# Performance work log

Hardware: AMD Instinct MI355X
Metric: run time of the kernel (lower is better)

## Reference

```python
import jax, jax.numpy as jnp
import numpy as np

EDGE = 255                      # env_edge_size
ADD = (EDGE - 1) // 2           # additional_size = 127
AX = EDGE + ADD                 # axial_size = 382 (input height H)
BATCH = 16
CHAN = 32


def setup_inputs() -> dict:
    key = jax.random.key(0)
    k1, k2 = jax.random.split(key)
    axial_tensor = jax.random.normal(k1, (BATCH, CHAN, AX, EDGE), dtype=jnp.float32)
    offset = jax.random.randint(k2, (BATCH, 2), 0, EDGE)  # (q, r) per batch
    return {"axial_tensor": axial_tensor, "offset": offset}


def reference(axial_tensor, offset):
    # Faithful translation of AxialTranslatorRotator.translate (translate=True path).
    B, C, H, W = axial_tensor.shape          # H = axial_size, W = edge_size
    add = H - W                              # additional_size
    S = 2 * H + 1                            # placeholder side = 2*axial_size + 1

    q = offset[:, 0]
    r = offset[:, 1]
    uoff = q - r // 2                        # us in torch code (floor div, r >= 0)

    # _axial_indices flatten order: loops over (u=i in [0,W), v=j in [0,H)),
    # flat index k = i*H + j; original gather reads x[b, c, j, i].
    j = jnp.arange(H)                        # v coordinate (indexes input H dim)
    i = jnp.arange(W)                        # u coordinate (indexes input W dim)

    # transformed indices: assigned_u = v - uoff + H - add ; assigned_v = u - r + H
    au = j[None, None, :] - uoff[:, None, None] + (H - add)   # (B, 1, H)
    av = i[None, :, None] - r[:, None, None] + H               # (B, W, 1)
    au = jnp.broadcast_to(au, (B, W, H)).reshape(B, W * H)
    av = jnp.broadcast_to(av, (B, W, H)).reshape(B, W * H)

    # values in matching flat order: vals[b, i*H + j, c] = x[b, c, j, i]
    vals = jnp.transpose(axial_tensor, (0, 3, 2, 1)).reshape(B, W * H, C)

    out = jnp.zeros((B, S, S, C), dtype=axial_tensor.dtype)
    out = out.at[jnp.arange(B)[:, None], au, av].set(vals, unique_indices=True)
    out = jnp.transpose(out, (0, 3, 1, 2))   # (B, C, S, S)

    # AxialMapBounds
    u_min = H - add - uoff
    v_min = H - r
    u_max = u_min + H
    v_max = v_min + W
    return out, u_min, u_max, v_min, v_max
```

## Files before the change

### kernel.cpp

```cpp
#include <hip/hip_runtime.h>

namespace {
constexpr int kB = 16;
constexpr int kC = 32;
constexpr int kH = 382;
constexpr int kW = 255;
constexpr int kS = 765;
constexpr unsigned kPlane = (unsigned)kS * (unsigned)kS;
constexpr unsigned long long kOutElems =
    (unsigned long long)kB * kC * (unsigned long long)kPlane;
constexpr unsigned kNVec = (unsigned)(kOutElems / 4ull);
}

__global__ __launch_bounds__(256) void axial_gather_kernel(
    const float* __restrict__ in, const int* __restrict__ off,
    float* __restrict__ out)
{
    unsigned t = blockIdx.x * 256u + threadIdx.x;
    if (t >= kNVec) return;
    unsigned idx = t * 4u;

    unsigned plane = idx / kPlane;
    unsigned rem   = idx - plane * kPlane;
    unsigned u     = rem / (unsigned)kS;
    unsigned v     = rem - u * (unsigned)kS;
    unsigned c     = plane & 31u;
    unsigned b     = plane >> 5;

    int q = off[2u * b];
    int r = off[2u * b + 1u];
    int du = (q - (r >> 1)) - 255;
    int dv = r - 382;

    float4 res;
    float* rp = reinterpret_cast<float*>(&res);

#pragma unroll
    for (int k = 0; k < 4; ++k) {
        int h = (int)u + du;
        int w = (int)v + dv;
        float val = 0.0f;
        if ((unsigned)h < (unsigned)kH && (unsigned)w < (unsigned)kW) {
            val = in[(((size_t)b * kC + c) * kH + (unsigned)h) * (size_t)kW
                     + (unsigned)w];
        }
        rp[k] = val;
        if (k < 3) {
            if (++v == (unsigned)kS) {
                v = 0u;
                if (++u == (unsigned)kS) {
                    u = 0u;
                    if (++c == (unsigned)kC) {
                        c = 0u;
                        ++b;
                        if (b < (unsigned)kB) {
                            q = off[2u * b];
                            r = off[2u * b + 1u];
                            du = (q - (r >> 1)) - 255;
                            dv = r - 382;
                        }
                    }
                }
            }
        }
    }
    reinterpret_cast<float4*>(out)[t] = res;
}

__global__ void axial_extras_kernel(const int* __restrict__ off,
                                    float* __restrict__ out_tail)
{
    int i = threadIdx.x;
    if (i >= 64) return;
    int b = i & 15;
    int which = i >> 4;
    int q = off[2 * b];
    int r = off[2 * b + 1];
    int uoff = q - (r >> 1);
    int u_min = 255 - uoff;
    int v_min = 382 - r;
    int val = (which == 0) ? u_min
            : (which == 1) ? (u_min + kH)
            : (which == 2) ? v_min
                           : (v_min + kW);
    out_tail[i] = (float)val;
}

extern "C" void kernel_launch(void* const* d_in, const int* in_sizes, int n_in,
                              void* d_out, int out_size, void* d_ws, size_t ws_size,
                              hipStream_t stream) {
    const float* in  = (const float*)d_in[0];
    const int*   off = (const int*)d_in[1];
    float*       out = (float*)d_out;

    unsigned blocks = (kNVec + 255u) / 256u;
    axial_gather_kernel<<<dim3(blocks), dim3(256), 0, stream>>>(in, off, out);
    axial_extras_kernel<<<dim3(1), dim3(64), 0, stream>>>(off, out + kOutElems);
}
```

Measured before the change: 385.7 us.

## Restructure gather into row-chunk blocks with per-plane offsets and scalar coalesced stores

Replaces the flat float4-per-thread gather, which decomposed every linear index with divisions and carried index increments, with blocks that each handle five output rows of one (batch, channel) plane. Per-block batch offsets and row validity are computed once, and threads stride across each row with scalar stores. This removes per-element index arithmetic and divergent carry logic but gives up 16-byte vector stores.

```diff
diff --git a/kernel.cpp b/kernel.cpp
--- a/kernel.cpp
+++ b/kernel.cpp
@@ -6,65 +6,52 @@
 constexpr int kH = 382;
 constexpr int kW = 255;
 constexpr int kS = 765;
-constexpr unsigned kPlane = (unsigned)kS * (unsigned)kS;
+constexpr int kRows = 5;
+constexpr int kChunks = kS / kRows;
+constexpr int kThreads = 192;
 constexpr unsigned long long kOutElems =
-    (unsigned long long)kB * kC * (unsigned long long)kPlane;
-constexpr unsigned kNVec = (unsigned)(kOutElems / 4ull);
+    (unsigned long long)kB * kC * (unsigned long long)kS * (unsigned long long)kS;
 }
 
-__global__ __launch_bounds__(256) void axial_gather_kernel(
+__global__ __launch_bounds__(kThreads) void axial_rows_kernel(
     const float* __restrict__ in, const int* __restrict__ off,
     float* __restrict__ out)
 {
-    unsigned t = blockIdx.x * 256u + threadIdx.x;
-    if (t >= kNVec) return;
-    unsigned idx = t * 4u;
-
-    unsigned plane = idx / kPlane;
-    unsigned rem   = idx - plane * kPlane;
-    unsigned u     = rem / (unsigned)kS;
-    unsigned v     = rem - u * (unsigned)kS;
-    unsigned c     = plane & 31u;
+    unsigned bid   = blockIdx.x;
+    unsigned chunk = bid % (unsigned)kChunks;
+    unsigned plane = bid / (unsigned)kChunks;
     unsigned b     = plane >> 5;
 
-    int q = off[2u * b];
-    int r = off[2u * b + 1u];
-    int du = (q - (r >> 1)) - 255;
-    int dv = r - 382;
+    int q   = off[2u * b];
+    int r   = off[2u * b + 1u];
+    int du  = (q - (r >> 1)) - 255;
+    int vlo = 382 - r;
+    int vhi = vlo + kW;
 
-    float4 res;
-    float* rp = reinterpret_cast<float*>(&res);
+    const float* inplane = in + (size_t)plane * (size_t)(kH * kW);
+    float* outchunk = out + (size_t)plane * (size_t)kS * (size_t)kS
+                          + (size_t)chunk * (size_t)(kRows * kS);
+
+    int t  = (int)threadIdx.x;
+    int u0 = (int)chunk * kRows;
 
 #pragma unroll
-    for (int k = 0; k < 4; ++k) {
-        int h = (int)u + du;
-        int w = (int)v + dv;
-        float val = 0.0f;
-        if ((unsigned)h < (unsigned)kH && (unsigned)w < (unsigned)kW) {
-            val = in[(((size_t)b * kC + c) * kH + (unsigned)h) * (size_t)kW
-                     + (unsigned)w];
-        }
-        rp[k] = val;
-        if (k < 3) {
-            if (++v == (unsigned)kS) {
-                v = 0u;
-                if (++u == (unsigned)kS) {
-                    u = 0u;
-                    if (++c == (unsigned)kC) {
-                        c = 0u;
-                        ++b;
-                        if (b < (unsigned)kB) {
-                            q = off[2u * b];
-                            r = off[2u * b + 1u];
-                            du = (q - (r >> 1)) - 255;
-                            dv = r - 382;
-                        }
-                    }
-                }
+    for (int i = 0; i < kRows; ++i) {
+        int h = u0 + i + du;
+        bool crow = ((unsigned)h < (unsigned)kH);
+        const float* inrow =
+            inplane + (ptrdiff_t)(crow ? h : 0) * kW - (ptrdiff_t)vlo;
+        float* outrow = outchunk + (size_t)i * kS;
+#pragma unroll
+        for (int j = 0; j < 4; ++j) {
+            int v = t + j * kThreads;
+            if (j < 3 || v < kS) {
+                float val = 0.0f;
+                if (crow && v >= vlo && v < vhi) val = inrow[v];
+                outrow[v] = val;
             }
         }
     }
-    reinterpret_cast<float4*>(out)[t] = res;
 }
 
 __global__ void axial_extras_kernel(const int* __restrict__ off,
@@ -93,7 +80,7 @@
     const int*   off = (const int*)d_in[1];
     float*       out = (float*)d_out;
 
-    unsigned blocks = (kNVec + 255u) / 256u;
-    axial_gather_kernel<<<dim3(blocks), dim3(256), 0, stream>>>(in, off, out);
+    unsigned blocks = (unsigned)(kB * kC * kChunks);
+    axial_rows_kernel<<<dim3(blocks), dim3(kThreads), 0, stream>>>(in, off, out);
     axial_extras_kernel<<<dim3(1), dim3(64), 0, stream>>>(off, out + kOutElems);
 }
```

Result: slower. 443.2 us (+14.9%).
